# Performance work log

Hardware: AMD Instinct MI355X
Metric: run time of the kernel (lower is better)

The kernel has to match this reference:

```python
import jax, jax.numpy as jnp
import numpy as np

DIM = 1024
NHEADS = 16
HEAD_DIM = DIM // NHEADS


def setup_inputs() -> dict:
    key = jax.random.key(0)
    ks = jax.random.split(key, 11)
    B, S = 4, 2048
    scale = 1.0 / np.sqrt(DIM)
    inp = {
        "Q": jax.random.normal(ks[0], (B, S, DIM), jnp.float32),
        "K": jax.random.normal(ks[1], (B, S, DIM), jnp.float32),
        "V": jax.random.normal(ks[2], (B, S, DIM), jnp.float32),
        "Wq": jax.random.normal(ks[3], (DIM, DIM), jnp.float32) * scale,
        "bq": jnp.zeros((DIM,), jnp.float32),
        "Wk": jax.random.normal(ks[4], (DIM, DIM), jnp.float32) * scale,
        "bk": jnp.zeros((DIM,), jnp.float32),
        "Wv": jax.random.normal(ks[5], (DIM, DIM), jnp.float32) * scale,
        "bv": jnp.zeros((DIM,), jnp.float32),
        "Wo": jax.random.normal(ks[6], (DIM, DIM), jnp.float32) * scale,
        "bo": jnp.zeros((DIM,), jnp.float32),
    }
    return inp


def _split_heads(x):
    # [B, S, D] -> [B, H, S, hd]
    B, S, _ = x.shape
    return x.reshape(B, S, NHEADS, HEAD_DIM).transpose(0, 2, 1, 3)


def reference(Q, K, V, Wq, bq, Wk, bk, Wv, bv, Wo, bo):
    q = _split_heads(Q @ Wq + bq)  # [B,H,S,hd]
    k = _split_heads(K @ Wk + bk)
    v = _split_heads(V @ Wv + bv)
    scores = jnp.einsum("bhqd,bhkd->bhqk", q, k) / np.sqrt(HEAD_DIM)
    attn = jax.nn.softmax(scores, axis=-1)  # dropout p=0 -> identity
    out = jnp.einsum("bhqk,bhkd->bhqd", attn, v)  # [B,H,S,hd]
    B, H, S, hd = out.shape
    out = out.transpose(0, 2, 1, 3).reshape(B, S, H * hd)
    return out @ Wo + bo
```

## Files before the change

kernel.cpp:

```cpp
#include <hip/hip_runtime.h>
#include <hip/hip_bf16.h>
#include <math.h>

#define DIM     1024
#define NHEADS  16
#define HD      64
#define BATCH   4
#define SEQ     2048
#define M_TOT   (BATCH * SEQ)
#define QSCALE  0.180336880111f

using short8 = __attribute__((ext_vector_type(8))) short;
using bf16x4 = __attribute__((ext_vector_type(4))) short;
using f32x4  = __attribute__((ext_vector_type(4))) float;

__device__ inline unsigned short f2bf(float x) {
    __hip_bfloat16 h = __float2bfloat16(x);
    unsigned short u;
    __builtin_memcpy(&u, &h, sizeof(u));
    return u;
}
__device__ inline void st_o(float* p, float v)          { *p = v; }
__device__ inline void st_o(unsigned short* p, float v) { *p = f2bf(v); }

__device__ inline void async16(const void* g, void* l) {
    __builtin_amdgcn_global_load_lds(
        (const __attribute__((address_space(1))) void*)g,
        (__attribute__((address_space(3))) void*)l, 16, 0, 0);
}

__global__ __launch_bounds__(256) void cvt3(
    const float* __restrict__ S0, const float* __restrict__ S1,
    const float* __restrict__ S2,
    unsigned short* __restrict__ D0, unsigned short* __restrict__ D1,
    unsigned short* __restrict__ D2)
{
    const float* src; unsigned short* dst;
    switch (blockIdx.y) {
        case 0:  src = S0; dst = D0; break;
        case 1:  src = S1; dst = D1; break;
        default: src = S2; dst = D2; break;
    }
    const size_t i = ((size_t)blockIdx.x * 256 + threadIdx.x) * 16;
    unsigned short tmp[16];
    #pragma unroll
    for (int p = 0; p < 4; ++p) {
        const float4 v = *(const float4*)(src + i + p * 4);
        tmp[p * 4 + 0] = f2bf(v.x); tmp[p * 4 + 1] = f2bf(v.y);
        tmp[p * 4 + 2] = f2bf(v.z); tmp[p * 4 + 3] = f2bf(v.w);
    }
    *(short8*)(dst + i)     = *(short8*)&tmp[0];
    *(short8*)(dst + i + 8) = *(short8*)&tmp[8];
}

__global__ __launch_bounds__(256) void wcvt4(
    const float* __restrict__ W0, const float* __restrict__ W1,
    const float* __restrict__ W2, const float* __restrict__ W3,
    unsigned short* __restrict__ T0, unsigned short* __restrict__ T1,
    unsigned short* __restrict__ T2, unsigned short* __restrict__ T3)
{
    const float* W; unsigned short* Wt;
    switch (blockIdx.z) {
        case 0:  W = W0; Wt = T0; break;
        case 1:  W = W1; Wt = T1; break;
        case 2:  W = W2; Wt = T2; break;
        default: W = W3; Wt = T3; break;
    }
    __shared__ unsigned short tile[32][33];
    const int t = threadIdx.x;
    const int tx = t & 31, ty = t >> 5;
    const int n0 = blockIdx.x * 32, k0 = blockIdx.y * 32;
    #pragma unroll
    for (int i = 0; i < 4; ++i) {
        const int kk = ty + i * 8;
        tile[kk][tx] = f2bf(W[(size_t)(k0 + kk) * DIM + n0 + tx]);
    }
    __syncthreads();
    #pragma unroll
    for (int i = 0; i < 4; ++i) {
        const int nn = ty + i * 8;
        Wt[(size_t)(n0 + nn) * DIM + k0 + tx] = tile[tx][nn];
    }
}

template <typename TY, bool TRANSV>
__device__ __forceinline__ void gemm_body(
    const unsigned short* A, const unsigned short* Wt,
    const float* bias, TY* Y, float scale,
    unsigned short* As, unsigned short* Bs)
{
    const int t = threadIdx.x;
    const int lane = t & 63, wv = t >> 6;
    const int wm = wv >> 1, wn = wv & 1;
    const int l16 = lane & 15, lq = lane >> 4;
    const int m0 = blockIdx.y * 128, n0 = blockIdx.x * 128;
    const int lrow = lane >> 2;
    const int lcol = (lane & 3) * 8;

    f32x4 acc[4][4] = {};

    #pragma unroll
    for (int c = 0; c < 2; ++c) {
        const int ci  = wv * 2 + c;
        const int row = ci * 16 + lrow;
        async16(A  + (size_t)(m0 + row) * DIM + lcol, &As[ci * 512]);
        async16(Wt + (size_t)(n0 + row) * DIM + lcol, &Bs[ci * 512]);
    }
    __syncthreads();

    int cur = 0;
    for (int k0 = 0; k0 < DIM; k0 += 32) {
        if (k0 + 32 < DIM) {
            unsigned short* Ad = As + (cur ^ 1) * 4096;
            unsigned short* Bd = Bs + (cur ^ 1) * 4096;
            #pragma unroll
            for (int c = 0; c < 2; ++c) {
                const int ci  = wv * 2 + c;
                const int row = ci * 16 + lrow;
                async16(A  + (size_t)(m0 + row) * DIM + k0 + 32 + lcol, Ad + ci * 512);
                async16(Wt + (size_t)(n0 + row) * DIM + k0 + 32 + lcol, Bd + ci * 512);
            }
        }
        const unsigned short* Ac = As + cur * 4096;
        const unsigned short* Bc = Bs + cur * 4096;

        short8 af[4], bfr[4];
        #pragma unroll
        for (int mi = 0; mi < 4; ++mi)
            af[mi] = *(const short8*)&Ac[(wm * 64 + mi * 16 + l16) * 32 + lq * 8];
        #pragma unroll
        for (int nj = 0; nj < 4; ++nj)
            bfr[nj] = *(const short8*)&Bc[(wn * 64 + nj * 16 + l16) * 32 + lq * 8];
        #pragma unroll
        for (int mi = 0; mi < 4; ++mi)
            #pragma unroll
            for (int nj = 0; nj < 4; ++nj)
                acc[mi][nj] = __builtin_amdgcn_mfma_f32_16x16x32_bf16(
                    af[mi], bfr[nj], acc[mi][nj], 0, 0, 0);

        __syncthreads();
        cur ^= 1;
    }

    #pragma unroll
    for (int mi = 0; mi < 4; ++mi)
        #pragma unroll
        for (int nj = 0; nj < 4; ++nj) {
            const int row = m0 + wm * 64 + mi * 16 + lq * 4;
            const int col = n0 + wn * 64 + nj * 16 + l16;
            const float bb = bias[col];
            if constexpr (TRANSV) {
                unsigned short o[4];
                #pragma unroll
                for (int r = 0; r < 4; ++r)
                    o[r] = f2bf((acc[mi][nj][r] + bb) * scale);
                const int bb_ = row >> 11, ss = row & (SEQ - 1);
                unsigned short* dst = (unsigned short*)Y +
                    ((size_t)(bb_ * NHEADS + (col >> 6)) * HD + (col & 63)) * SEQ + ss;
                *(bf16x4*)dst = *(const bf16x4*)o;
            } else {
                #pragma unroll
                for (int r = 0; r < 4; ++r)
                    st_o(&Y[(size_t)(row + r) * DIM + col],
                         (acc[mi][nj][r] + bb) * scale);
            }
        }
}

template <typename TY, bool TRANSV = false>
__global__ __launch_bounds__(256) void gemm_a16(
    const unsigned short* __restrict__ A, const unsigned short* __restrict__ Wt,
    const float* __restrict__ bias, TY* __restrict__ Y, float scale)
{
    __shared__ unsigned short As[2 * 128 * 32];
    __shared__ unsigned short Bs[2 * 128 * 32];
    gemm_body<TY, TRANSV>(A, Wt, bias, Y, scale, As, Bs);
}

__global__ __launch_bounds__(256) void gemm_qk(
    const unsigned short* Aq, const unsigned short* Wtq, const float* bq_,
    unsigned short* Yq,
    const unsigned short* Ak, const unsigned short* Wtk, const float* bk_,
    unsigned short* Yk)
{
    __shared__ unsigned short As[2 * 128 * 32];
    __shared__ unsigned short Bs[2 * 128 * 32];
    const bool k = blockIdx.z != 0;
    gemm_body<unsigned short, false>(k ? Ak : Aq, k ? Wtk : Wtq, k ? bk_ : bq_,
                                     k ? Yk : Yq, k ? 1.0f : QSCALE, As, Bs);
}

__global__ __launch_bounds__(256) void attn_mfma(
    const unsigned short* qbuf, const unsigned short* __restrict__ kbuf,
    const unsigned short* __restrict__ vtb, unsigned short* ctx)
{
    __shared__ unsigned short Kls[2 * 64 * 64];
    __shared__ unsigned short Vls[2 * 64 * 64];

    const int t = threadIdx.x;
    const int lane = t & 63, wv = t >> 6;
    const int l16 = lane & 15, lq = lane >> 4;
    const int l7 = l16 & 7;
    const int lqh = lq >> 1, lql4 = (lq & 1) * 4;

    const unsigned lin  = (blockIdx.z * gridDim.y + blockIdx.y) * gridDim.x + blockIdx.x;
    const unsigned xcd  = lin & 7, slot = lin >> 3;
    const unsigned bh   = ((slot >> 5) << 3) | xcd;
    const int b = (int)(bh >> 4), h = (int)(bh & 15);
    const int q0 = (int)(slot & 31) * 64;

    const size_t base  = ((size_t)b * SEQ) * DIM + h * HD;
    const size_t vbase = ((size_t)(b * NHEADS + h)) * HD * SEQ;

    const int rl   = lane >> 3;
    const int gcol = ((lane & 7) ^ rl) << 3;

    {
        const int r = t >> 2, c = (t & 3) * 16;
        const int g0 = c >> 3, rx = r & 7;
        const unsigned short* src = qbuf + base + (size_t)(q0 + r) * DIM + c;
        *(short8*)&Kls[r * 64 + ((g0 ^ rx) << 3)]       = *(const short8*)src;
        *(short8*)&Kls[r * 64 + (((g0 + 1) ^ rx) << 3)] = *(const short8*)(src + 8);
    }
    const int qrow = wv * 16 + l16;
    const short8 qf0 = *(const short8*)&Kls[qrow * 64 + ((lq ^ l7) << 3)];
    const short8 qf1 = *(const short8*)&Kls[qrow * 64 + (((4 + lq) ^ l7) << 3)];
    asm volatile("" :: "v"(qf0), "v"(qf1));
    __syncthreads();

    float l_acc = 0.f;
    f32x4 O[4] = {};

    #pragma unroll
    for (int c = 0; c < 2; ++c) {
        const int ci = wv * 2 + c;
        async16(kbuf + base + (size_t)(ci * 8 + rl) * DIM + gcol, Kls + ci * 512);
        async16(vtb + vbase + (size_t)(ci * 8 + rl) * SEQ + gcol, Vls + ci * 512);
    }
    __syncthreads();

    int cur = 0;
    for (int s0 = 0; s0 < SEQ; s0 += 64) {
        const unsigned short* Kc = Kls + cur * 4096;
        const unsigned short* Vc = Vls + cur * 4096;

        if (s0 + 64 < SEQ) {
            unsigned short* Kd = Kls + (cur ^ 1) * 4096;
            unsigned short* Vd = Vls + (cur ^ 1) * 4096;
            #pragma unroll
            for (int c = 0; c < 2; ++c) {
                const int ci = wv * 2 + c;
                async16(kbuf + base + (size_t)(s0 + 64 + ci * 8 + rl) * DIM + gcol,
                        Kd + ci * 512);
                async16(vtb + vbase + (size_t)(ci * 8 + rl) * SEQ + s0 + 64 + gcol,
                        Vd + ci * 512);
            }
        }

        f32x4 sa[4] = {};
        #pragma unroll
        for (int ti = 0; ti < 4; ++ti) {
            const int rr = ti * 16 + l16;
            const short8 kf0 = *(const short8*)(Kc + rr * 64 + ((lq ^ l7) << 3));
            const short8 kf1 = *(const short8*)(Kc + rr * 64 + (((4 + lq) ^ l7) << 3));
            sa[ti] = __builtin_amdgcn_mfma_f32_16x16x32_bf16(kf0, qf0, sa[ti], 0, 0, 0);
            sa[ti] = __builtin_amdgcn_mfma_f32_16x16x32_bf16(kf1, qf1, sa[ti], 0, 0, 0);
        }

        #pragma unroll
        for (int ti = 0; ti < 4; ++ti) {
            const float v0 = __builtin_amdgcn_exp2f(sa[ti][0]);
            const float v1 = __builtin_amdgcn_exp2f(sa[ti][1]);
            const float v2 = __builtin_amdgcn_exp2f(sa[ti][2]);
            const float v3 = __builtin_amdgcn_exp2f(sa[ti][3]);
            l_acc += (v0 + v1) + (v2 + v3);
            bf16x4 pa;
            pa[0] = (short)f2bf(v0); pa[1] = (short)f2bf(v1);
            pa[2] = (short)f2bf(v2); pa[3] = (short)f2bf(v3);
            #pragma unroll
            for (int dt = 0; dt < 4; ++dt) {
                const int vr = dt * 16 + l16;
                const bf16x4 vb = *(const bf16x4*)(
                    Vc + vr * 64 + (((2 * ti + lqh) ^ l7) << 3) + lql4);
                O[dt] = __builtin_amdgcn_mfma_f32_16x16x16bf16_1k(pa, vb, O[dt], 0, 0, 0);
            }
        }

        __syncthreads();
        cur ^= 1;
    }

    l_acc += __shfl_xor(l_acc, 16);
    l_acc += __shfl_xor(l_acc, 32);

    unsigned short (*Ol)[72] = (unsigned short(*)[72])Kls;
    #pragma unroll
    for (int r = 0; r < 4; ++r) {
        const float inv = 1.0f / __shfl(l_acc, lq * 4 + r);
        const int orow = wv * 16 + lq * 4 + r;
        #pragma unroll
        for (int dt = 0; dt < 4; ++dt)
            Ol[orow][dt * 16 + l16] = f2bf(O[dt][r] * inv);
    }
    __syncthreads();
    {
        const int r = t >> 2, c = (t & 3) * 16;
        unsigned short* dst = ctx + base + (size_t)(q0 + r) * DIM + c;
        *(short8*)dst       = *(const short8*)&Ol[r][c];
        *(short8*)(dst + 8) = *(const short8*)&Ol[r][c + 8];
    }
}

extern "C" void kernel_launch(void* const* d_in, const int* in_sizes, int n_in,
                              void* d_out, int out_size, void* d_ws, size_t ws_size,
                              hipStream_t stream) {
    const float* Q  = (const float*)d_in[0];
    const float* K  = (const float*)d_in[1];
    const float* V  = (const float*)d_in[2];
    const float* Wq = (const float*)d_in[3];
    const float* bq = (const float*)d_in[4];
    const float* Wk = (const float*)d_in[5];
    const float* bk = (const float*)d_in[6];
    const float* Wv = (const float*)d_in[7];
    const float* bv = (const float*)d_in[8];
    const float* Wo = (const float*)d_in[9];
    const float* bo = (const float*)d_in[10];
    float* out = (float*)d_out;

    const size_t eW = (size_t)DIM * DIM;
    const size_t eB = (size_t)M_TOT * DIM;
    unsigned short* p   = (unsigned short*)d_ws;
    unsigned short* wtq = p; p += eW;
    unsigned short* wtk = p; p += eW;
    unsigned short* wtv = p; p += eW;
    unsigned short* wto = p; p += eW;
    unsigned short* bufA = p; p += eB;
    unsigned short* bufB = p; p += eB;
    unsigned short* bufC = p; p += eB;
    unsigned short* bufD = p; p += eB;
    unsigned short* bufE = p;

    wcvt4<<<dim3(32, 32, 4), 256, 0, stream>>>(Wq, Wk, Wv, Wo, wtq, wtk, wtv, wto);

    const int cvt_blocks = (int)(eB / (256 * 16));
    cvt3<<<dim3(cvt_blocks, 3), 256, 0, stream>>>(V, Q, K, bufA, bufC, bufB);

    const dim3 gg(DIM / 128, M_TOT / 128);

    gemm_a16<unsigned short, true><<<gg, 256, 0, stream>>>(
        bufA, wtv, bv, bufE, 1.0f);
    gemm_qk<<<dim3(DIM / 128, M_TOT / 128, 2), 256, 0, stream>>>(
        bufC, wtq, bq, bufA,
        bufB, wtk, bk, bufD);

    attn_mfma<<<dim3(SEQ / 64, NHEADS, BATCH), 256, 0, stream>>>(bufA, bufD, bufE, bufA);

    gemm_a16<float><<<gg, 256, 0, stream>>>(bufA, wto, bo, out, 1.0f);
}
```

Baseline: 383.8 us.

## Fuse V projection into QK GEMM launch and stage Q in separate LDS

Merges the V projection GEMM into the Q/K projection kernel as a third z-slice, so one launch with more blocks replaces two. Q output now goes into the final output buffer used as scratch, which lets the attention kernel read Q from a buffer that does not alias its ctx output and mark everything __restrict__. Q is staged in a dedicated LDS buffer, removing a __syncthreads at the cost of extra shared memory that may lower occupancy. P-to-bf16 conversion is replaced with a cheaper packed rounding (add 0x8000, truncate) that drops NaN handling and round-to-nearest-even.

After: 374.3 us. 1.03x faster.

```diff
diff --git a/kernel.cpp b/kernel.cpp
--- a/kernel.cpp
+++ b/kernel.cpp
@@ -22,6 +22,13 @@
 }
 __device__ inline void st_o(float* p, float v)          { *p = v; }
 __device__ inline void st_o(unsigned short* p, float v) { *p = f2bf(v); }
+
+__device__ inline unsigned pk2bf(float a, float b) {
+    unsigned ua, ub;
+    __builtin_memcpy(&ua, &a, 4); __builtin_memcpy(&ub, &b, 4);
+    ua += 0x8000u; ub += 0x8000u;
+    return (ua >> 16) | (ub & 0xffff0000u);
+}
 
 __device__ inline void async16(const void* g, void* l) {
     __builtin_amdgcn_global_load_lds(
@@ -177,7 +184,9 @@
     gemm_body<TY, TRANSV>(A, Wt, bias, Y, scale, As, Bs);
 }
 
-__global__ __launch_bounds__(256) void gemm_qk(
+__global__ __launch_bounds__(256) void gemm_qkv(
+    const unsigned short* Av, const unsigned short* Wtv, const float* bv_,
+    unsigned short* Yv,
     const unsigned short* Aq, const unsigned short* Wtq, const float* bq_,
     unsigned short* Yq,
     const unsigned short* Ak, const unsigned short* Wtk, const float* bk_,
@@ -185,17 +194,22 @@
 {
     __shared__ unsigned short As[2 * 128 * 32];
     __shared__ unsigned short Bs[2 * 128 * 32];
-    const bool k = blockIdx.z != 0;
-    gemm_body<unsigned short, false>(k ? Ak : Aq, k ? Wtk : Wtq, k ? bk_ : bq_,
-                                     k ? Yk : Yq, k ? 1.0f : QSCALE, As, Bs);
+    const int z = blockIdx.z;
+    if (z == 0)
+        gemm_body<unsigned short, true >(Av, Wtv, bv_, Yv, 1.0f,   As, Bs);
+    else if (z == 1)
+        gemm_body<unsigned short, false>(Aq, Wtq, bq_, Yq, QSCALE, As, Bs);
+    else
+        gemm_body<unsigned short, false>(Ak, Wtk, bk_, Yk, 1.0f,   As, Bs);
 }
 
 __global__ __launch_bounds__(256) void attn_mfma(
-    const unsigned short* qbuf, const unsigned short* __restrict__ kbuf,
-    const unsigned short* __restrict__ vtb, unsigned short* ctx)
+    const unsigned short* __restrict__ qbuf, const unsigned short* __restrict__ kbuf,
+    const unsigned short* __restrict__ vtb, unsigned short* __restrict__ ctx)
 {
     __shared__ unsigned short Kls[2 * 64 * 64];
     __shared__ unsigned short Vls[2 * 64 * 64];
+    __shared__ unsigned short Qls[64 * 64];
 
     const int t = threadIdx.x;
     const int lane = t & 63, wv = t >> 6;
@@ -219,14 +233,12 @@
         const int r = t >> 2, c = (t & 3) * 16;
         const int g0 = c >> 3, rx = r & 7;
         const unsigned short* src = qbuf + base + (size_t)(q0 + r) * DIM + c;
-        *(short8*)&Kls[r * 64 + ((g0 ^ rx) << 3)]       = *(const short8*)src;
-        *(short8*)&Kls[r * 64 + (((g0 + 1) ^ rx) << 3)] = *(const short8*)(src + 8);
+        *(short8*)&Qls[r * 64 + ((g0 ^ rx) << 3)]       = *(const short8*)src;
+        *(short8*)&Qls[r * 64 + (((g0 + 1) ^ rx) << 3)] = *(const short8*)(src + 8);
     }
     const int qrow = wv * 16 + l16;
-    const short8 qf0 = *(const short8*)&Kls[qrow * 64 + ((lq ^ l7) << 3)];
-    const short8 qf1 = *(const short8*)&Kls[qrow * 64 + (((4 + lq) ^ l7) << 3)];
-    asm volatile("" :: "v"(qf0), "v"(qf1));
-    __syncthreads();
+    const short8 qf0 = *(const short8*)&Qls[qrow * 64 + ((lq ^ l7) << 3)];
+    const short8 qf1 = *(const short8*)&Qls[qrow * 64 + (((4 + lq) ^ l7) << 3)];
 
     float l_acc = 0.f;
     f32x4 O[4] = {};
@@ -274,9 +286,9 @@
             const float v2 = __builtin_amdgcn_exp2f(sa[ti][2]);
             const float v3 = __builtin_amdgcn_exp2f(sa[ti][3]);
             l_acc += (v0 + v1) + (v2 + v3);
+            unsigned pw[2] = { pk2bf(v0, v1), pk2bf(v2, v3) };
             bf16x4 pa;
-            pa[0] = (short)f2bf(v0); pa[1] = (short)f2bf(v1);
-            pa[2] = (short)f2bf(v2); pa[3] = (short)f2bf(v3);
+            __builtin_memcpy(&pa, pw, 8);
             #pragma unroll
             for (int dt = 0; dt < 4; ++dt) {
                 const int vr = dt * 16 + l16;
@@ -339,21 +351,20 @@
     unsigned short* bufC = p; p += eB;
     unsigned short* bufD = p; p += eB;
     unsigned short* bufE = p;
+    unsigned short* qfs = (unsigned short*)out;
 
     wcvt4<<<dim3(32, 32, 4), 256, 0, stream>>>(Wq, Wk, Wv, Wo, wtq, wtk, wtv, wto);
 
     const int cvt_blocks = (int)(eB / (256 * 16));
     cvt3<<<dim3(cvt_blocks, 3), 256, 0, stream>>>(V, Q, K, bufA, bufC, bufB);
 
-    const dim3 gg(DIM / 128, M_TOT / 128);
-
-    gemm_a16<unsigned short, true><<<gg, 256, 0, stream>>>(
-        bufA, wtv, bv, bufE, 1.0f);
-    gemm_qk<<<dim3(DIM / 128, M_TOT / 128, 2), 256, 0, stream>>>(
-        bufC, wtq, bq, bufA,
+    gemm_qkv<<<dim3(DIM / 128, M_TOT / 128, 3), 256, 0, stream>>>(
+        bufA, wtv, bv, bufE,
+        bufC, wtq, bq, qfs,
         bufB, wtk, bk, bufD);
 
-    attn_mfma<<<dim3(SEQ / 64, NHEADS, BATCH), 256, 0, stream>>>(bufA, bufD, bufE, bufA);
-
-    gemm_a16<float><<<gg, 256, 0, stream>>>(bufA, wto, bo, out, 1.0f);
-}
+    attn_mfma<<<dim3(SEQ / 64, NHEADS, BATCH), 256, 0, stream>>>(qfs, bufD, bufE, bufA);
+
+    gemm_a16<float><<<dim3(DIM / 128, M_TOT / 128), 256, 0, stream>>>(
+        bufA, wto, bo, out, 1.0f);
+}
```
